# Kernel optimization log

Measured on AMD Instinct MI355X. Metric: run time of the kernel, lower is better.

Reference implementation:

```python
import jax, jax.numpy as jnp
import numpy as np

B, S, E = 2, 2048, 1024
H, D = 16, 64
BASE = 10000.0


def rotate_half(x):
    x1, x2 = jnp.split(x, 2, axis=-1)
    return jnp.concatenate((-x2, x1), axis=-1)


def rope_cos_sin(seq_len, dim):
    inv_freq = 1.0 / (BASE ** (jnp.arange(0, dim, 2, dtype=jnp.float32) / dim))
    t = jnp.arange(seq_len, dtype=jnp.float32)
    freqs = jnp.einsum('i,j->ij', t, inv_freq)          # [S, D/2]
    emb = jnp.concatenate((freqs, freqs), axis=-1)       # [S, D]
    return jnp.cos(emb), jnp.sin(emb)


def setup_inputs() -> dict:
    key = jax.random.key(0)
    ks = jax.random.split(key, 9)
    s = 1.0 / np.sqrt(E)
    inp = {
        'x': jax.random.normal(ks[0], (B, S, E), dtype=jnp.float32),
        'mask': jnp.ones((B, S), dtype=jnp.int32),
        'Wq': jax.random.normal(ks[1], (E, H * D), dtype=jnp.float32) * s,
        'bq': jnp.zeros((H * D,), dtype=jnp.float32),
        'Wk': jax.random.normal(ks[2], (E, H * D), dtype=jnp.float32) * s,
        'bk': jnp.zeros((H * D,), dtype=jnp.float32),
        'Wv': jax.random.normal(ks[3], (E, H * D), dtype=jnp.float32) * s,
        'bv': jnp.zeros((H * D,), dtype=jnp.float32),
        'Wo': jax.random.normal(ks[4], (H * D, E), dtype=jnp.float32) * s,
        'bo': jnp.zeros((E,), dtype=jnp.float32),
    }
    return inp


def reference(x, mask, Wq, bq, Wk, bk, Wv, bv, Wo, bo):
    b, s, _ = x.shape
    scale = D ** (-0.5)
    # projections -> [B, H, S, D]
    q = (x @ Wq + bq).reshape(b, s, H, D).transpose(0, 2, 1, 3)
    k = (x @ Wk + bk).reshape(b, s, H, D).transpose(0, 2, 1, 3)
    v = (x @ Wv + bv).reshape(b, s, H, D).transpose(0, 2, 1, 3)
    # rotary position embedding
    cos, sin = rope_cos_sin(s, D)                      # [S, D]
    cos = cos[None, None]
    sin = sin[None, None]
    q = q * cos + rotate_half(q) * sin
    k = k * cos + rotate_half(k) * sin
    # scores [B, H, S, S]
    scores = jnp.einsum('bhqd,bhkd->bhqk', q, k) * scale
    # padding mask [B,1,1,S]
    scores = jnp.where(mask[:, None, None, :] == 0, -jnp.inf, scores)
    # causal mask
    i = jnp.arange(s)
    causal = jnp.where(i[None, :] > i[:, None], -jnp.inf, 0.0)  # [S, S]
    scores = scores + causal[None, None]
    attn = jax.nn.softmax(scores, axis=-1)
    ctx = jnp.einsum('bhqk,bhkd->bhqd', attn, v)
    ctx = ctx.transpose(0, 2, 1, 3).reshape(b, s, H * D)
    return ctx @ Wo + bo
```

## Files before the change

kernel.cpp:

```cpp
#include <hip/hip_runtime.h>
#include <cstdint>
#include <cstddef>

#define DEVI __device__ __forceinline__

typedef __bf16 bf16_t;
typedef __bf16 bf16x4 __attribute__((ext_vector_type(4)));
typedef __bf16 bf16x8 __attribute__((ext_vector_type(8)));
typedef float  f32x4  __attribute__((ext_vector_type(4)));
typedef float  f32x16 __attribute__((ext_vector_type(16)));
typedef unsigned short u16x4 __attribute__((ext_vector_type(4)));

static constexpr int Bz = 2, S = 2048, E = 1024, H = 16, Dh = 64;
static constexpr int M  = Bz * S;
static constexpr int N  = H * Dh;
static constexpr int Kd = E;

DEVI unsigned short f2bf(float f) {
  unsigned u = __builtin_bit_cast(unsigned, f);
  return (unsigned short)((u + 0x7fffu + ((u >> 16) & 1u)) >> 16);
}

DEVI void async_copy16(void* lds, const void* g) {
  __builtin_amdgcn_global_load_lds((__attribute__((address_space(1))) void*)(g),
                                   (__attribute__((address_space(3))) void*)(lds), 16, 0, 0);
}

__global__ void prep_kernel(const float* __restrict__ x, bf16_t* __restrict__ xb,
                            const float* __restrict__ Wq, const float* __restrict__ Wk,
                            const float* __restrict__ Wv, const float* __restrict__ Wo,
                            bf16_t* __restrict__ WtBase,
                            float* __restrict__ ropeC, float* __restrict__ ropeS) {
  __shared__ unsigned short tile[64][68];
  const int blk = blockIdx.x, tid = threadIdx.x;
  if (blk < 4096) {
    int i = blk * 256 + tid;
    float4 v = ((const float4*)x)[i];
    u16x4 o = { f2bf(v.x), f2bf(v.y), f2bf(v.z), f2bf(v.w) };
    ((u16x4*)xb)[i] = o;
  } else if (blk < 5120) {
    const int i = blk - 4096;
    const int z = i >> 8, rest = i & 255;
    const int n0 = (rest & 15) * 64, k0 = (rest >> 4) * 64;
    const float* W = (z == 0) ? Wq : (z == 1) ? Wk : (z == 2) ? Wv : Wo;
    unsigned short* T = (unsigned short*)(WtBase + (size_t)z * Kd * N);
    for (int e = tid; e < 1024; e += 256) {
      int r = e >> 4, c4 = (e & 15) * 4;
      float4 v = *(const float4*)(W + (size_t)(k0 + r) * N + n0 + c4);
      u16x4 o = { f2bf(v.x), f2bf(v.y), f2bf(v.z), f2bf(v.w) };
      *(u16x4*)&tile[r][c4] = o;
    }
    __syncthreads();
    for (int e = tid; e < 1024; e += 256) {
      int r = e >> 4, c4 = (e & 15) * 4;
      u16x4 o = { tile[c4][r], tile[c4 + 1][r], tile[c4 + 2][r], tile[c4 + 3][r] };
      *(u16x4*)&T[(size_t)(n0 + r) * Kd + k0 + c4] = o;
    }
  } else {
    int i = (blk - 5120) * 256 + tid;
    int pos = i >> 5, j = i & 31;
    float inv = exp2f(-(float)j * 0.41524101186092029f);
    float ang = (float)pos * inv;
    ropeC[i] = cosf(ang);
    ropeS[i] = sinf(ang);
  }
}

__global__ void vtrans_kernel(const bf16_t* __restrict__ V, bf16_t* __restrict__ Vt) {
  __shared__ unsigned short tile[64][68];
  const int bh = blockIdx.y;
  const int s0 = blockIdx.x * 64;
  const unsigned short* Vp = (const unsigned short*)V + (size_t)bh * S * Dh;
  unsigned short* Tp = (unsigned short*)Vt + (size_t)bh * Dh * S;
  const int tid = threadIdx.x;
  for (int e = tid; e < 1024; e += 256) {
    int r = e >> 4, c4 = (e & 15) * 4;
    u16x4 v = *(const u16x4*)(Vp + (size_t)(s0 + r) * Dh + c4);
    *(u16x4*)&tile[r][c4] = v;
  }
  __syncthreads();
  for (int e = tid; e < 1024; e += 256) {
    int d = e >> 4, s4 = (e & 15) * 4;
    u16x4 o = { tile[s4][d], tile[s4 + 1][d], tile[s4 + 2][d], tile[s4 + 3][d] };
    *(u16x4*)&Tp[(size_t)d * S + s0 + s4] = o;
  }
}


DEVI void gemm_mainloop(const bf16_t* __restrict__ A, const bf16_t* __restrict__ Bt,
                        bf16_t* sA, bf16_t* sB, int m0, int n0, f32x4 (&acc)[4][4]) {
  const int tid  = threadIdx.x;
  const int lane = tid & 63;
  const int wid  = tid >> 6;
  const int l16  = lane & 15;
  const int quad = lane >> 4;
  const int wm = (wid >> 1) * 64;
  const int wn = (wid & 1) * 64;
  const int o0 = wid * 2048 + lane * 16;
  const int o1 = o0 + 1024;
  const int r0 = o0 >> 6, c0 = o0 & 63;
  const int r1 = o1 >> 6, c1 = o1 & 63;
  const char* Ab = (const char*)A;
  const char* Bb = (const char*)Bt;
  char* sAc = (char*)sA;
  char* sBc = (char*)sB;

  auto stage = [&](int buf, int k0) {
    async_copy16(sAc + buf * 8192 + wid * 2048,        Ab + ((size_t)(m0 + r0) * Kd + k0) * 2 + c0);
    async_copy16(sAc + buf * 8192 + wid * 2048 + 1024, Ab + ((size_t)(m0 + r1) * Kd + k0) * 2 + c1);
    async_copy16(sBc + buf * 8192 + wid * 2048,        Bb + ((size_t)(n0 + r0) * Kd + k0) * 2 + c0);
    async_copy16(sBc + buf * 8192 + wid * 2048 + 1024, Bb + ((size_t)(n0 + r1) * Kd + k0) * 2 + c1);
  };

  stage(0, 0);
  for (int i = 0; i < Kd / 32; ++i) {
    __syncthreads();
    if (i + 1 < Kd / 32) stage((i + 1) & 1, (i + 1) * 32);
    const bf16_t* a = sA + (i & 1) * 4096;
    const bf16_t* b = sB + (i & 1) * 4096;
    bf16x8 af[4], bfv[4];
#pragma unroll
    for (int mi = 0; mi < 4; ++mi)
      af[mi] = *(const bf16x8*)(a + (wm + mi * 16 + l16) * 32 + quad * 8);
#pragma unroll
    for (int ni = 0; ni < 4; ++ni)
      bfv[ni] = *(const bf16x8*)(b + (wn + ni * 16 + l16) * 32 + quad * 8);
#pragma unroll
    for (int mi = 0; mi < 4; ++mi)
#pragma unroll
      for (int ni = 0; ni < 4; ++ni)
        acc[mi][ni] = __builtin_amdgcn_mfma_f32_16x16x32_bf16(af[mi], bfv[ni], acc[mi][ni], 0, 0, 0);
  }
}

__global__ __launch_bounds__(256, 3) void gemm_qkv_kernel(
    const bf16_t* __restrict__ xb, const bf16_t* __restrict__ WtBase,
    const float* __restrict__ bq, const float* __restrict__ bk, const float* __restrict__ bv,
    bf16_t* __restrict__ outBase,
    const float* __restrict__ ropeC, const float* __restrict__ ropeS) {
  __shared__ bf16_t sA[2][4096], sB[2][4096];
  const int z = blockIdx.z;
  const bf16_t* Bt = WtBase + (size_t)z * Kd * N;
  const float* bias = (z == 0) ? bq : (z == 1) ? bk : bv;
  unsigned short* outp = (unsigned short*)(outBase + (size_t)z * M * N);
  const int n0 = blockIdx.x * 128, m0 = blockIdx.y * 128;
  f32x4 acc[4][4] = {};
  gemm_mainloop(xb, Bt, &sA[0][0], &sB[0][0], m0, n0, acc);

  const int tid = threadIdx.x, lane = tid & 63, wid = tid >> 6;
  const int l16 = lane & 15, quad = lane >> 4;
  const int wm = (wid >> 1) * 64, wn = (wid & 1) * 64;
  const int cbase = n0 + wn;
  const int h = cbase >> 6;

  if (z < 2) {
    const float qs = (z == 0) ? 0.18033688011112042f : 1.0f;
#pragma unroll
    for (int mi = 0; mi < 4; ++mi)
#pragma unroll
      for (int r = 0; r < 4; ++r) {
        int t = m0 + wm + mi * 16 + quad * 4 + r;
        int bb = t >> 11, s = t & (S - 1);
        size_t obase = ((size_t)(bb * H + h) * S + s) * Dh;
#pragma unroll
        for (int np = 0; np < 2; ++np) {
          int j = np * 16 + l16;
          float cc = ropeC[s * 32 + j];
          float ss = ropeS[s * 32 + j];
          float xlo = acc[mi][np][r]     + bias[cbase + j];
          float xhi = acc[mi][np + 2][r] + bias[cbase + j + 32];
          outp[obase + j]      = f2bf((xlo * cc - xhi * ss) * qs);
          outp[obase + j + 32] = f2bf((xhi * cc + xlo * ss) * qs);
        }
      }
  } else {
#pragma unroll
    for (int mi = 0; mi < 4; ++mi)
#pragma unroll
      for (int r = 0; r < 4; ++r) {
        int t = m0 + wm + mi * 16 + quad * 4 + r;
        int bb = t >> 11, s = t & (S - 1);
        size_t obase = ((size_t)(bb * H + h) * S + s) * Dh;
#pragma unroll
        for (int ni = 0; ni < 4; ++ni) {
          int d = ni * 16 + l16;
          outp[obase + d] = f2bf(acc[mi][ni][r] + bias[cbase + d]);
        }
      }
  }
}

__global__ __launch_bounds__(256, 4) void gemm_o_kernel(
    const bf16_t* __restrict__ A, const bf16_t* __restrict__ Bt,
    const float* __restrict__ bias, float* __restrict__ out) {
  __shared__ bf16_t sA[2][2048], sB[2][4096];
  const int n0 = blockIdx.x * 128, m0 = blockIdx.y * 64;
  const int tid = threadIdx.x, lane = tid & 63, wid = tid >> 6;
  const int l16 = lane & 15, quad = lane >> 4;
  const int wm = (wid >> 1) * 32, wn = (wid & 1) * 64;
  const int rowoff = lane >> 2, col8 = (lane & 3) * 8;
  const char* Ab = (const char*)A;
  const char* Bb = (const char*)Bt;
  char* sAc = (char*)sA;
  char* sBc = (char*)sB;
  f32x4 acc[2][4] = {};

  auto stage = [&](int buf, int k0) {
    async_copy16(sAc + buf * 4096 + wid * 1024,
                 Ab + ((size_t)(m0 + wid * 16 + rowoff) * Kd + k0 + col8) * 2);
    async_copy16(sBc + buf * 8192 + (wid * 2) * 1024,
                 Bb + ((size_t)(n0 + wid * 32 + rowoff) * Kd + k0 + col8) * 2);
    async_copy16(sBc + buf * 8192 + (wid * 2 + 1) * 1024,
                 Bb + ((size_t)(n0 + wid * 32 + 16 + rowoff) * Kd + k0 + col8) * 2);
  };

  stage(0, 0);
  for (int i = 0; i < Kd / 32; ++i) {
    __syncthreads();
    if (i + 1 < Kd / 32) stage((i + 1) & 1, (i + 1) * 32);
    const bf16_t* a = &sA[0][0] + (i & 1) * 2048;
    const bf16_t* b = &sB[0][0] + (i & 1) * 4096;
    bf16x8 af[2], bfv[4];
#pragma unroll
    for (int mi = 0; mi < 2; ++mi)
      af[mi] = *(const bf16x8*)(a + (wm + mi * 16 + l16) * 32 + quad * 8);
#pragma unroll
    for (int ni = 0; ni < 4; ++ni)
      bfv[ni] = *(const bf16x8*)(b + (wn + ni * 16 + l16) * 32 + quad * 8);
#pragma unroll
    for (int mi = 0; mi < 2; ++mi)
#pragma unroll
      for (int ni = 0; ni < 4; ++ni)
        acc[mi][ni] = __builtin_amdgcn_mfma_f32_16x16x32_bf16(af[mi], bfv[ni], acc[mi][ni], 0, 0, 0);
  }
#pragma unroll
  for (int mi = 0; mi < 2; ++mi)
#pragma unroll
    for (int r = 0; r < 4; ++r) {
      int t = m0 + wm + mi * 16 + quad * 4 + r;
#pragma unroll
      for (int ni = 0; ni < 4; ++ni) {
        int c = n0 + wn + ni * 16 + l16;
        out[(size_t)t * N + c] = acc[mi][ni][r] + bias[c];
      }
    }
}

__global__ __launch_bounds__(256, 3) void attn_kernel(
    const bf16_t* __restrict__ Q, const bf16_t* __restrict__ Kb,
    const bf16_t* __restrict__ Vt, const int* __restrict__ mask,
    bf16_t* __restrict__ ctx) {
  __shared__ bf16_t sK[2][4096];
  __shared__ bf16_t sV[2][4096];
  __shared__ unsigned short sP[4][32 * 72];

  const int tid = threadIdx.x, lane = tid & 63, wid = tid >> 6;
  const int l32 = lane & 31, half = lane >> 5;

  const int idx  = blockIdx.x;
  const int qblk = 15 - (idx >> 5);
  const int bh   = idx & 31;
  const int b    = bh >> 4;
  const int q0   = qblk * 128;
  const int qw   = q0 + wid * 32;

  const bf16_t* Qp = Q + ((size_t)bh * S + qw) * Dh;
  const char*   Kg = (const char*)(Kb + (size_t)bh * S * Dh);
  const char*   Vg = (const char*)(Vt + (size_t)bh * Dh * S);
  const int*    mp = mask + b * S;

  bf16x8 qf[4];
#pragma unroll
  for (int c = 0; c < 4; ++c)
    qf[c] = *(const bf16x8*)(Qp + l32 * Dh + c * 16 + half * 8);

  const int ks0 = wid * 2, ks1 = wid * 2 + 1;
  const size_t kOff0 = (((size_t)((ks0 >> 2) * 32 + l32)) * Dh + (ks0 & 3) * 16 + half * 8) * 2;
  const size_t kOff1 = (((size_t)((ks1 >> 2) * 32 + l32)) * Dh + (ks1 & 3) * 16 + half * 8) * 2;
  const size_t vOff0 = (((size_t)((ks0 >> 2) * 32 + l32)) * S  + (ks0 & 3) * 16 + half * 8) * 2;
  const size_t vOff1 = (((size_t)((ks1 >> 2) * 32 + l32)) * S  + (ks1 & 3) * 16 + half * 8) * 2;
  char* sKc = (char*)sK;
  char* sVc = (char*)sV;

  auto stage = [&](int buf, int kt) {
    size_t kbK = (size_t)kt * 64 * Dh * 2;
    size_t kbV = (size_t)kt * 64 * 2;
    async_copy16(sKc + buf * 8192 + ks0 * 1024, Kg + kbK + kOff0);
    async_copy16(sKc + buf * 8192 + ks1 * 1024, Kg + kbK + kOff1);
    async_copy16(sVc + buf * 8192 + ks0 * 1024, Vg + kbV + vOff0);
    async_copy16(sVc + buf * 8192 + ks1 * 1024, Vg + kbV + vOff1);
  };

  f32x16 cacc[2] = {};
  float lsum = 0.f;
  const int qcol = qw + l32;
  const int niter = 2 * (qblk + 1);
  unsigned short* pb = &sP[wid][0];

  stage(0, 0);
  for (int kt = 0; kt < niter; ++kt) {
    const int kb = kt * 64;
    __syncthreads();
    if (kt + 1 < niter) stage((kt + 1) & 1, kt + 1);
    if (kb <= qw + 31) {
      int mk = mp[kb + lane];
      const bf16_t* kbuf = &sK[kt & 1][0];
      const bf16_t* vbuf = &sV[kt & 1][0];

      f32x16 st[2] = {};
#pragma unroll
      for (int g = 0; g < 2; ++g)
#pragma unroll
        for (int c = 0; c < 4; ++c) {
          bf16x8 kf = *(const bf16x8*)(kbuf + (g * 4 + c) * 512 + lane * 8);
          st[g] = __builtin_amdgcn_mfma_f32_32x32x16_bf16(kf, qf[c], st[g], 0, 0, 0);
        }

      unsigned long long dm = __ballot(mk == 0);
      if (dm) {
#pragma unroll
        for (int g = 0; g < 2; ++g)
#pragma unroll
          for (int r = 0; r < 16; ++r) {
            int krow = g * 32 + (r & 3) + 8 * (r >> 2) + 4 * half;
            if ((dm >> krow) & 1ull) st[g][r] = -1e30f;
          }
      }
      if (kb + 63 > qw) {
#pragma unroll
        for (int g = 0; g < 2; ++g)
#pragma unroll
          for (int r = 0; r < 16; ++r) {
            int key = kb + g * 32 + (r & 3) + 8 * (r >> 2) + 4 * half;
            if (key > qcol) st[g][r] = -1e30f;
          }
      }

#pragma unroll
      for (int g = 0; g < 2; ++g)
#pragma unroll
        for (int rg = 0; rg < 4; ++rg) {
          float e0 = exp2f(st[g][rg * 4 + 0]);
          float e1 = exp2f(st[g][rg * 4 + 1]);
          float e2 = exp2f(st[g][rg * 4 + 2]);
          float e3 = exp2f(st[g][rg * 4 + 3]);
          lsum += (e0 + e1) + (e2 + e3);
          bf16x4 pk = { (bf16_t)e0, (bf16_t)e1, (bf16_t)e2, (bf16_t)e3 };
          *(bf16x4*)&pb[l32 * 72 + g * 32 + rg * 8 + half * 4] = pk;
        }

      bf16x8 pf[4];
#pragma unroll
      for (int c = 0; c < 4; ++c)
        pf[c] = *(const bf16x8*)((const bf16_t*)(const void*)pb + l32 * 72 + c * 16 + half * 8);

#pragma unroll
      for (int dg = 0; dg < 2; ++dg)
#pragma unroll
        for (int c = 0; c < 4; ++c) {
          bf16x8 vf = *(const bf16x8*)(vbuf + (dg * 4 + c) * 512 + lane * 8);
          cacc[dg] = __builtin_amdgcn_mfma_f32_32x32x16_bf16(pf[c], vf, cacc[dg], 0, 0, 0);
        }
    }
  }

  lsum += __shfl_xor(lsum, 32);
  float iv = 1.0f / lsum;
  float* ib = (float*)(void*)pb;
  if (half == 0) ib[l32] = iv;
  f32x4 ivq[4];
#pragma unroll
  for (int rg = 0; rg < 4; ++rg)
    ivq[rg] = *(const f32x4*)&ib[rg * 8 + half * 4];

  unsigned short* cp = (unsigned short*)ctx;
  const size_t base = ((size_t)(b * S + qw)) * N + (size_t)(bh & 15) * 64;
#pragma unroll
  for (int dg = 0; dg < 2; ++dg)
#pragma unroll
    for (int r = 0; r < 16; ++r) {
      int row = (r & 3) + 8 * (r >> 2) + 4 * half;
      cp[base + (size_t)row * N + dg * 32 + l32] = f2bf(cacc[dg][r] * ivq[r >> 2][r & 3]);
    }
}


extern "C" void kernel_launch(void* const* d_in, const int* in_sizes, int n_in,
                              void* d_out, int out_size, void* d_ws, size_t ws_size,
                              hipStream_t stream) {
  const float* x  = (const float*)d_in[0];
  const int*  msk = (const int*)d_in[1];
  const float* Wq = (const float*)d_in[2];
  const float* bq = (const float*)d_in[3];
  const float* Wk = (const float*)d_in[4];
  const float* bk = (const float*)d_in[5];
  const float* Wv = (const float*)d_in[6];
  const float* bv = (const float*)d_in[7];
  const float* Wo = (const float*)d_in[8];
  const float* bo = (const float*)d_in[9];
  float* out = (float*)d_out;
  (void)in_sizes; (void)n_in; (void)out_size; (void)ws_size;

  char* ws = (char*)d_ws;
  bf16_t* xb   = (bf16_t*)(ws);
  bf16_t* WT   = (bf16_t*)(ws + (8u  << 20));
  bf16_t* qkv  = (bf16_t*)(ws + (16u << 20));
  bf16_t* Qb   = qkv;
  bf16_t* Kbuf = qkv + (size_t)1 * M * N;
  bf16_t* Vb   = qkv + (size_t)2 * M * N;
  bf16_t* Vt   = xb;
  bf16_t* ctx  = Vb;
  float* ropeC = (float*)(ws + (40u << 20));
  float* ropeS = ropeC + (size_t)S * 32;

  prep_kernel<<<5376, 256, 0, stream>>>(x, xb, Wq, Wk, Wv, Wo, WT, ropeC, ropeS);
  gemm_qkv_kernel<<<dim3(8, 32, 3), 256, 0, stream>>>(xb, WT, bq, bk, bv, qkv, ropeC, ropeS);
  vtrans_kernel<<<dim3(32, 32), 256, 0, stream>>>(Vb, Vt);
  attn_kernel<<<512, 256, 0, stream>>>(Qb, Kbuf, Vt, msk, ctx);
  gemm_o_kernel<<<dim3(8, 64), 256, 0, stream>>>(ctx, WT + (size_t)3 * Kd * N, bo, out);
}
```

Before: 216.2 us.

## Drop LDS double buffering in GEMMs and load K/V directly from global in attention

Both GEMM main loops go from double-buffered async LDS staging to single-buffered staging with a barrier before and after each load. This halves shared memory per block but exposes load latency on every k-step. The attention kernel drops LDS staging of K and V entirely and reads fragments straight from global memory. It also remaps blocks so each wave owns a different head over a 32-row query tile, removing block-level barriers and the idle waves of the causal triangle. This trades shared-memory reuse across the four waves for per-wave global (cache) traffic.

```diff
diff --git a/kernel.cpp b/kernel.cpp
--- a/kernel.cpp
+++ b/kernel.cpp
@@ -105,26 +105,20 @@
   char* sAc = (char*)sA;
   char* sBc = (char*)sB;
 
-  auto stage = [&](int buf, int k0) {
-    async_copy16(sAc + buf * 8192 + wid * 2048,        Ab + ((size_t)(m0 + r0) * Kd + k0) * 2 + c0);
-    async_copy16(sAc + buf * 8192 + wid * 2048 + 1024, Ab + ((size_t)(m0 + r1) * Kd + k0) * 2 + c1);
-    async_copy16(sBc + buf * 8192 + wid * 2048,        Bb + ((size_t)(n0 + r0) * Kd + k0) * 2 + c0);
-    async_copy16(sBc + buf * 8192 + wid * 2048 + 1024, Bb + ((size_t)(n0 + r1) * Kd + k0) * 2 + c1);
-  };
-
-  stage(0, 0);
-  for (int i = 0; i < Kd / 32; ++i) {
-    __syncthreads();
-    if (i + 1 < Kd / 32) stage((i + 1) & 1, (i + 1) * 32);
-    const bf16_t* a = sA + (i & 1) * 4096;
-    const bf16_t* b = sB + (i & 1) * 4096;
+  for (int k0 = 0; k0 < Kd; k0 += 32) {
+    __syncthreads();
+    async_copy16(sAc + wid * 2048,        Ab + ((size_t)(m0 + r0) * Kd + k0) * 2 + c0);
+    async_copy16(sAc + wid * 2048 + 1024, Ab + ((size_t)(m0 + r1) * Kd + k0) * 2 + c1);
+    async_copy16(sBc + wid * 2048,        Bb + ((size_t)(n0 + r0) * Kd + k0) * 2 + c0);
+    async_copy16(sBc + wid * 2048 + 1024, Bb + ((size_t)(n0 + r1) * Kd + k0) * 2 + c1);
+    __syncthreads();
     bf16x8 af[4], bfv[4];
 #pragma unroll
     for (int mi = 0; mi < 4; ++mi)
-      af[mi] = *(const bf16x8*)(a + (wm + mi * 16 + l16) * 32 + quad * 8);
+      af[mi] = *(const bf16x8*)(sA + (wm + mi * 16 + l16) * 32 + quad * 8);
 #pragma unroll
     for (int ni = 0; ni < 4; ++ni)
-      bfv[ni] = *(const bf16x8*)(b + (wn + ni * 16 + l16) * 32 + quad * 8);
+      bfv[ni] = *(const bf16x8*)(sB + (wn + ni * 16 + l16) * 32 + quad * 8);
 #pragma unroll
     for (int mi = 0; mi < 4; ++mi)
 #pragma unroll
@@ -138,14 +132,14 @@
     const float* __restrict__ bq, const float* __restrict__ bk, const float* __restrict__ bv,
     bf16_t* __restrict__ outBase,
     const float* __restrict__ ropeC, const float* __restrict__ ropeS) {
-  __shared__ bf16_t sA[2][4096], sB[2][4096];
+  __shared__ bf16_t sA[4096], sB[4096];
   const int z = blockIdx.z;
   const bf16_t* Bt = WtBase + (size_t)z * Kd * N;
   const float* bias = (z == 0) ? bq : (z == 1) ? bk : bv;
   unsigned short* outp = (unsigned short*)(outBase + (size_t)z * M * N);
   const int n0 = blockIdx.x * 128, m0 = blockIdx.y * 128;
   f32x4 acc[4][4] = {};
-  gemm_mainloop(xb, Bt, &sA[0][0], &sB[0][0], m0, n0, acc);
+  gemm_mainloop(xb, Bt, sA, sB, m0, n0, acc);
 
   const int tid = threadIdx.x, lane = tid & 63, wid = tid >> 6;
   const int l16 = lane & 15, quad = lane >> 4;
@@ -193,7 +187,7 @@
 __global__ __launch_bounds__(256, 4) void gemm_o_kernel(
     const bf16_t* __restrict__ A, const bf16_t* __restrict__ Bt,
     const float* __restrict__ bias, float* __restrict__ out) {
-  __shared__ bf16_t sA[2][2048], sB[2][4096];
+  __shared__ bf16_t sA[2048], sB[4096];
   const int n0 = blockIdx.x * 128, m0 = blockIdx.y * 64;
   const int tid = threadIdx.x, lane = tid & 63, wid = tid >> 6;
   const int l16 = lane & 15, quad = lane >> 4;
@@ -205,28 +199,22 @@
   char* sBc = (char*)sB;
   f32x4 acc[2][4] = {};
 
-  auto stage = [&](int buf, int k0) {
-    async_copy16(sAc + buf * 4096 + wid * 1024,
+  for (int k0 = 0; k0 < Kd; k0 += 32) {
+    __syncthreads();
+    async_copy16(sAc + wid * 1024,
                  Ab + ((size_t)(m0 + wid * 16 + rowoff) * Kd + k0 + col8) * 2);
-    async_copy16(sBc + buf * 8192 + (wid * 2) * 1024,
+    async_copy16(sBc + (wid * 2) * 1024,
                  Bb + ((size_t)(n0 + wid * 32 + rowoff) * Kd + k0 + col8) * 2);
-    async_copy16(sBc + buf * 8192 + (wid * 2 + 1) * 1024,
+    async_copy16(sBc + (wid * 2 + 1) * 1024,
                  Bb + ((size_t)(n0 + wid * 32 + 16 + rowoff) * Kd + k0 + col8) * 2);
-  };
-
-  stage(0, 0);
-  for (int i = 0; i < Kd / 32; ++i) {
-    __syncthreads();
-    if (i + 1 < Kd / 32) stage((i + 1) & 1, (i + 1) * 32);
-    const bf16_t* a = &sA[0][0] + (i & 1) * 2048;
-    const bf16_t* b = &sB[0][0] + (i & 1) * 4096;
+    __syncthreads();
     bf16x8 af[2], bfv[4];
 #pragma unroll
     for (int mi = 0; mi < 2; ++mi)
-      af[mi] = *(const bf16x8*)(a + (wm + mi * 16 + l16) * 32 + quad * 8);
+      af[mi] = *(const bf16x8*)(sA + (wm + mi * 16 + l16) * 32 + quad * 8);
 #pragma unroll
     for (int ni = 0; ni < 4; ++ni)
-      bfv[ni] = *(const bf16x8*)(b + (wn + ni * 16 + l16) * 32 + quad * 8);
+      bfv[ni] = *(const bf16x8*)(sB + (wn + ni * 16 + l16) * 32 + quad * 8);
 #pragma unroll
     for (int mi = 0; mi < 2; ++mi)
 #pragma unroll
@@ -246,121 +234,93 @@
     }
 }
 
-__global__ __launch_bounds__(256, 3) void attn_kernel(
+__global__ __launch_bounds__(256) void attn_kernel(
     const bf16_t* __restrict__ Q, const bf16_t* __restrict__ Kb,
     const bf16_t* __restrict__ Vt, const int* __restrict__ mask,
     bf16_t* __restrict__ ctx) {
-  __shared__ bf16_t sK[2][4096];
-  __shared__ bf16_t sV[2][4096];
   __shared__ unsigned short sP[4][32 * 72];
 
   const int tid = threadIdx.x, lane = tid & 63, wid = tid >> 6;
   const int l32 = lane & 31, half = lane >> 5;
 
-  const int idx  = blockIdx.x;
-  const int qblk = 15 - (idx >> 5);
-  const int bh   = idx & 31;
-  const int b    = bh >> 4;
-  const int q0   = qblk * 128;
-  const int qw   = q0 + wid * 32;
-
-  const bf16_t* Qp = Q + ((size_t)bh * S + qw) * Dh;
-  const char*   Kg = (const char*)(Kb + (size_t)bh * S * Dh);
-  const char*   Vg = (const char*)(Vt + (size_t)bh * Dh * S);
+  const int qt = 63 - (blockIdx.x >> 3);
+  const int bh = ((blockIdx.x & 7) << 2) | wid;
+  const int b  = bh >> 4;
+  const int qw = qt * 32;
+
+  const bf16_t* Qp = Q  + ((size_t)bh * S + qw) * Dh;
+  const bf16_t* Kp = Kb + (size_t)bh * S * Dh;
+  const bf16_t* Vp = Vt + (size_t)bh * Dh * S;
   const int*    mp = mask + b * S;
 
   bf16x8 qf[4];
 #pragma unroll
   for (int c = 0; c < 4; ++c)
     qf[c] = *(const bf16x8*)(Qp + l32 * Dh + c * 16 + half * 8);
-
-  const int ks0 = wid * 2, ks1 = wid * 2 + 1;
-  const size_t kOff0 = (((size_t)((ks0 >> 2) * 32 + l32)) * Dh + (ks0 & 3) * 16 + half * 8) * 2;
-  const size_t kOff1 = (((size_t)((ks1 >> 2) * 32 + l32)) * Dh + (ks1 & 3) * 16 + half * 8) * 2;
-  const size_t vOff0 = (((size_t)((ks0 >> 2) * 32 + l32)) * S  + (ks0 & 3) * 16 + half * 8) * 2;
-  const size_t vOff1 = (((size_t)((ks1 >> 2) * 32 + l32)) * S  + (ks1 & 3) * 16 + half * 8) * 2;
-  char* sKc = (char*)sK;
-  char* sVc = (char*)sV;
-
-  auto stage = [&](int buf, int kt) {
-    size_t kbK = (size_t)kt * 64 * Dh * 2;
-    size_t kbV = (size_t)kt * 64 * 2;
-    async_copy16(sKc + buf * 8192 + ks0 * 1024, Kg + kbK + kOff0);
-    async_copy16(sKc + buf * 8192 + ks1 * 1024, Kg + kbK + kOff1);
-    async_copy16(sVc + buf * 8192 + ks0 * 1024, Vg + kbV + vOff0);
-    async_copy16(sVc + buf * 8192 + ks1 * 1024, Vg + kbV + vOff1);
-  };
 
   f32x16 cacc[2] = {};
   float lsum = 0.f;
   const int qcol = qw + l32;
-  const int niter = 2 * (qblk + 1);
+  const int niter = (qt >> 1) + 1;
   unsigned short* pb = &sP[wid][0];
 
-  stage(0, 0);
   for (int kt = 0; kt < niter; ++kt) {
     const int kb = kt * 64;
-    __syncthreads();
-    if (kt + 1 < niter) stage((kt + 1) & 1, kt + 1);
-    if (kb <= qw + 31) {
-      int mk = mp[kb + lane];
-      const bf16_t* kbuf = &sK[kt & 1][0];
-      const bf16_t* vbuf = &sV[kt & 1][0];
-
-      f32x16 st[2] = {};
+    int mk = mp[kb + lane];
+
+    f32x16 st[2] = {};
+#pragma unroll
+    for (int c = 0; c < 4; ++c) {
+      bf16x8 kf0 = *(const bf16x8*)(Kp + (size_t)(kb + l32) * Dh + c * 16 + half * 8);
+      bf16x8 kf1 = *(const bf16x8*)(Kp + (size_t)(kb + 32 + l32) * Dh + c * 16 + half * 8);
+      st[0] = __builtin_amdgcn_mfma_f32_32x32x16_bf16(kf0, qf[c], st[0], 0, 0, 0);
+      st[1] = __builtin_amdgcn_mfma_f32_32x32x16_bf16(kf1, qf[c], st[1], 0, 0, 0);
+    }
+
+    unsigned long long dm = __ballot(mk == 0);
+    if (dm) {
 #pragma unroll
       for (int g = 0; g < 2; ++g)
 #pragma unroll
-        for (int c = 0; c < 4; ++c) {
-          bf16x8 kf = *(const bf16x8*)(kbuf + (g * 4 + c) * 512 + lane * 8);
-          st[g] = __builtin_amdgcn_mfma_f32_32x32x16_bf16(kf, qf[c], st[g], 0, 0, 0);
+        for (int r = 0; r < 16; ++r) {
+          int krow = g * 32 + (r & 3) + 8 * (r >> 2) + 4 * half;
+          if ((dm >> krow) & 1ull) st[g][r] = -1e30f;
         }
-
-      unsigned long long dm = __ballot(mk == 0);
-      if (dm) {
-#pragma unroll
-        for (int g = 0; g < 2; ++g)
-#pragma unroll
-          for (int r = 0; r < 16; ++r) {
-            int krow = g * 32 + (r & 3) + 8 * (r >> 2) + 4 * half;
-            if ((dm >> krow) & 1ull) st[g][r] = -1e30f;
-          }
+    }
+    if (kt == niter - 1) {
+#pragma unroll
+      for (int g = 0; g < 2; ++g)
+#pragma unroll
+        for (int r = 0; r < 16; ++r) {
+          int key = kb + g * 32 + (r & 3) + 8 * (r >> 2) + 4 * half;
+          if (key > qcol) st[g][r] = -1e30f;
+        }
+    }
+
+#pragma unroll
+    for (int g = 0; g < 2; ++g)
+#pragma unroll
+      for (int rg = 0; rg < 4; ++rg) {
+        float e0 = exp2f(st[g][rg * 4 + 0]);
+        float e1 = exp2f(st[g][rg * 4 + 1]);
+        float e2 = exp2f(st[g][rg * 4 + 2]);
+        float e3 = exp2f(st[g][rg * 4 + 3]);
+        lsum += (e0 + e1) + (e2 + e3);
+        bf16x4 pk = { (bf16_t)e0, (bf16_t)e1, (bf16_t)e2, (bf16_t)e3 };
+        *(bf16x4*)&pb[l32 * 72 + g * 32 + rg * 8 + half * 4] = pk;
       }
-      if (kb + 63 > qw) {
-#pragma unroll
-        for (int g = 0; g < 2; ++g)
-#pragma unroll
-          for (int r = 0; r < 16; ++r) {
-            int key = kb + g * 32 + (r & 3) + 8 * (r >> 2) + 4 * half;
-            if (key > qcol) st[g][r] = -1e30f;
-          }
-      }
-
-#pragma unroll
-      for (int g = 0; g < 2; ++g)
-#pragma unroll
-        for (int rg = 0; rg < 4; ++rg) {
-          float e0 = exp2f(st[g][rg * 4 + 0]);
-          float e1 = exp2f(st[g][rg * 4 + 1]);
-          float e2 = exp2f(st[g][rg * 4 + 2]);
-          float e3 = exp2f(st[g][rg * 4 + 3]);
-          lsum += (e0 + e1) + (e2 + e3);
-          bf16x4 pk = { (bf16_t)e0, (bf16_t)e1, (bf16_t)e2, (bf16_t)e3 };
-          *(bf16x4*)&pb[l32 * 72 + g * 32 + rg * 8 + half * 4] = pk;
-        }
-
-      bf16x8 pf[4];
-#pragma unroll
-      for (int c = 0; c < 4; ++c)
-        pf[c] = *(const bf16x8*)((const bf16_t*)(const void*)pb + l32 * 72 + c * 16 + half * 8);
-
-#pragma unroll
-      for (int dg = 0; dg < 2; ++dg)
-#pragma unroll
-        for (int c = 0; c < 4; ++c) {
-          bf16x8 vf = *(const bf16x8*)(vbuf + (dg * 4 + c) * 512 + lane * 8);
-          cacc[dg] = __builtin_amdgcn_mfma_f32_32x32x16_bf16(pf[c], vf, cacc[dg], 0, 0, 0);
-        }
+
+    bf16x8 pf[4];
+#pragma unroll
+    for (int c = 0; c < 4; ++c)
+      pf[c] = *(const bf16x8*)((const bf16_t*)(const void*)pb + l32 * 72 + c * 16 + half * 8);
+
+#pragma unroll
+    for (int c = 0; c < 4; ++c) {
+      bf16x8 vf0 = *(const bf16x8*)(Vp + (size_t)l32 * S + kb + c * 16 + half * 8);
+      bf16x8 vf1 = *(const bf16x8*)(Vp + (size_t)(32 + l32) * S + kb + c * 16 + half * 8);
+      cacc[0] = __builtin_amdgcn_mfma_f32_32x32x16_bf16(pf[c], vf0, cacc[0], 0, 0, 0);
+      cacc[1] = __builtin_amdgcn_mfma_f32_32x32x16_bf16(pf[c], vf1, cacc[1], 0, 0, 0);
     }
   }
 
```

Result: slower. 242.4 us (+12.1%).
